# Kernel optimization log

Hardware: AMD Instinct MI355X
Metric: run time of the kernel (lower is better)

## Reference

```python
import jax, jax.numpy as jnp
import numpy as np

B, T, E, H = 2, 2048, 1024, 16
Dh = E // H  # head_size = 64


def setup_inputs() -> dict:
    key = jax.random.key(0)
    ks = jax.random.split(key, 6)
    s = E ** -0.5
    x = jax.random.normal(ks[0], (B, T, E), dtype=jnp.float32)
    Wq = jax.random.normal(ks[1], (H, E, Dh), dtype=jnp.float32) * s
    Wk = jax.random.normal(ks[2], (H, E, Dh), dtype=jnp.float32) * s
    Wv = jax.random.normal(ks[3], (H, E, Dh), dtype=jnp.float32) * s
    wo_w = jax.random.normal(ks[4], (E, E), dtype=jnp.float32) * s  # torch Linear weight [out,in]
    wo_b = jax.random.normal(ks[5], (E,), dtype=jnp.float32) * 0.01
    return {"x": x, "Wq": Wq, "Wk": Wk, "Wv": Wv, "wo_w": wo_w, "wo_b": wo_b}


def reference(x, Wq, Wk, Wv, wo_w, wo_b):
    # Batched equivalent of the per-head Python loop: project all heads at once.
    q = jnp.einsum('bte,hed->bhtd', x, Wq)
    k = jnp.einsum('bte,hed->bhtd', x, Wk)
    v = jnp.einsum('bte,hed->bhtd', x, Wv)
    scale = Dh ** -0.5
    scores = jnp.einsum('bhtd,bhsd->bhts', q, k) * scale  # [B,H,T,T]
    causal = jnp.tril(jnp.ones((T, T), dtype=bool))
    scores = jnp.where(causal, scores, jnp.finfo(scores.dtype).min)
    att = jax.nn.softmax(scores, axis=-1)
    out = jnp.einsum('bhts,bhsd->bhtd', att, v)  # [B,H,T,Dh]
    # concat heads (head order along last dim, matching torch.cat over heads)
    out = out.transpose(0, 2, 1, 3).reshape(B, T, E)
    return out @ wo_w.T + wo_b
```

## Files before the change

### kernel.cpp

```cpp
#include <hip/hip_runtime.h>

#define B_ 2
#define T_ 2048
#define E_ 1024
#define H_ 16
#define DH 64

typedef unsigned short u16;
typedef unsigned int u32;
typedef __bf16 bf16x8 __attribute__((ext_vector_type(8)));
typedef float f32x4 __attribute__((ext_vector_type(4)));
typedef float f32x16 __attribute__((ext_vector_type(16)));

__device__ __forceinline__ u16 f2bf(float f) {
  u32 u = __builtin_bit_cast(u32, f);
  u = u + 0x7FFFu + ((u >> 16) & 1u);
  return (u16)(u >> 16);
}
__device__ __forceinline__ bf16x8 ldfrag(const u16* p) { return *(const bf16x8*)p; }

__device__ __forceinline__ void gload_lds16(const u16* g, u16* l) {
  __builtin_amdgcn_global_load_lds((const __attribute__((address_space(1))) u32*)g,
                                   (__attribute__((address_space(3))) u32*)l, 16, 0, 0);
}

__global__ __launch_bounds__(256) void k_conv_all(const float* __restrict__ x,
                                                  const float* __restrict__ Wq,
                                                  const float* __restrict__ Wk,
                                                  const float* __restrict__ Wv,
                                                  const float* __restrict__ wo_w,
                                                  u16* __restrict__ xb, u16* __restrict__ wT,
                                                  u16* __restrict__ woB) {
  __shared__ __align__(16) u16 Ls[64][68];
  const int t = threadIdx.x;
  const int bx = blockIdx.x;
  if (bx < 2048 || bx >= 2816) {
    const float* src = (bx < 2048) ? x : wo_w;
    u16* dst = (bx < 2048) ? xb : woB;
    u32 i = (((bx < 2048) ? bx : (bx - 2816)) * 256u + t) * 8u;
    float4 a = *(const float4*)(src + i);
    float4 b = *(const float4*)(src + i + 4);
    uint4 v;
    v.x = (u32)f2bf(a.x) | ((u32)f2bf(a.y) << 16);
    v.y = (u32)f2bf(a.z) | ((u32)f2bf(a.w) << 16);
    v.z = (u32)f2bf(b.x) | ((u32)f2bf(b.y) << 16);
    v.w = (u32)f2bf(b.z) | ((u32)f2bf(b.w) << 16);
    *(uint4*)(dst + i) = v;
    return;
  }
  const int idx = bx - 2048;
  const int e0 = (idx & 15) * 64;
  const int h = (idx >> 4) & 15;
  const int which = idx >> 8;
  const float* src = (which == 0) ? Wq : ((which == 1) ? Wk : Wv);
  const float scale = (which == 0) ? 0.18033688011112042f : 1.0f;
#pragma unroll
  for (int p = 0; p < 4; p++) {
    int id2 = p * 256 + t;
    int row = id2 >> 4, ch = id2 & 15;
    float4 v = *(const float4*)(src + ((size_t)h * E_ + e0 + row) * DH + ch * 4);
    uint2 pk;
    pk.x = (u32)f2bf(v.x * scale) | ((u32)f2bf(v.y * scale) << 16);
    pk.y = (u32)f2bf(v.z * scale) | ((u32)f2bf(v.w * scale) << 16);
    *(uint2*)(&Ls[row][ch * 4]) = pk;
  }
  __syncthreads();
  u16* dst = wT + ((size_t)which * H_ + h) * (DH * E_);
#pragma unroll
  for (int p = 0; p < 4; p++) {
    int id2 = p * 256 + t;
    int d = id2 >> 4, ec = id2 & 15;
    uint2 pk;
    pk.x = (u32)Ls[ec * 4 + 0][d] | ((u32)Ls[ec * 4 + 1][d] << 16);
    pk.y = (u32)Ls[ec * 4 + 2][d] | ((u32)Ls[ec * 4 + 3][d] << 16);
    *(uint2*)(dst + (size_t)d * E_ + e0 + ec * 4) = pk;
  }
}

__global__ __launch_bounds__(256, 3) void k_qkv(const u16* __restrict__ xb, const u16* __restrict__ wT,
                                                u16* __restrict__ Qb, u16* __restrict__ Kb,
                                                u16* __restrict__ VbT) {
  __shared__ __align__(16) u16 As[128 * 64];
  __shared__ __align__(16) u16 Bs[128 * 64];
  const int tid = threadIdx.x;
  const int w = tid >> 6, lane = tid & 63, quad = lane >> 4, lr = lane & 15;
  const int wr = w >> 1, wc = w & 1;
  const int bid = blockIdx.x;
  const int xcd = bid & 7, bidx = bid >> 3;
  const int t0 = (xcd * 4 + bidx / 24) * 128;
  const int n0 = (bidx % 24) * 128;
  const int sr = lane >> 3, sc = lane & 7;

  f32x4 acc[4][4];
  const f32x4 z4 = {0.f, 0.f, 0.f, 0.f};
#pragma unroll
  for (int i = 0; i < 4; i++)
#pragma unroll
    for (int j = 0; j < 4; j++) acc[i][j] = z4;

  for (int k0 = 0; k0 < E_; k0 += 64) {
    __syncthreads();
#pragma unroll
    for (int ii = 0; ii < 4; ii++) {
      int ra = w * 32 + ii * 8 + sr;
      gload_lds16(xb + (size_t)(t0 + ra) * E_ + k0 + ((sc ^ (ra & 7)) << 3),
                  As + (w * 32 + ii * 8) * 64);
      gload_lds16(wT + (size_t)(n0 + ra) * E_ + k0 + ((sc ^ (ra & 7)) << 3),
                  Bs + (w * 32 + ii * 8) * 64);
    }
    __syncthreads();
#pragma unroll
    for (int kk = 0; kk < 2; kk++) {
      bf16x8 af[4], bfv[4];
#pragma unroll
      for (int rt = 0; rt < 4; rt++) {
        int row = wr * 64 + rt * 16 + lr;
        af[rt] = ldfrag(As + row * 64 + (((kk * 4 + quad) ^ (row & 7)) << 3));
      }
#pragma unroll
      for (int ct = 0; ct < 4; ct++) {
        int row = wc * 64 + ct * 16 + lr;
        bfv[ct] = ldfrag(Bs + row * 64 + (((kk * 4 + quad) ^ (row & 7)) << 3));
      }
#pragma unroll
      for (int rt = 0; rt < 4; rt++)
#pragma unroll
        for (int ct = 0; ct < 4; ct++)
          acc[rt][ct] = __builtin_amdgcn_mfma_f32_16x16x32_bf16(af[rt], bfv[ct], acc[rt][ct], 0, 0, 0);
    }
  }

  const int qkv = n0 >> 10;
  if (qkv < 2) {
    u16* outp = (qkv == 0) ? Qb : Kb;
#pragma unroll
    for (int rt = 0; rt < 4; rt++)
#pragma unroll
      for (int ct = 0; ct < 4; ct++) {
        int n = n0 + wc * 64 + ct * 16 + lr;
        int h = (n >> 6) & 15, d = n & 63;
#pragma unroll
        for (int r = 0; r < 4; r++) {
          int t = t0 + wr * 64 + rt * 16 + quad * 4 + r;
          int bb = t >> 11, tt = t & 2047;
          outp[(((size_t)bb * H_ + h) * T_ + tt) * DH + d] = f2bf(acc[rt][ct][r]);
        }
      }
  } else {
#pragma unroll
    for (int rt = 0; rt < 4; rt++)
#pragma unroll
      for (int ct = 0; ct < 4; ct++) {
        int n = n0 + wc * 64 + ct * 16 + lr;
        int h = (n >> 6) & 15, d = n & 63;
        int t = t0 + wr * 64 + rt * 16 + quad * 4;
        int bb = t >> 11, tt = t & 2047;
        uint2 pk;
        pk.x = (u32)f2bf(acc[rt][ct][0]) | ((u32)f2bf(acc[rt][ct][1]) << 16);
        pk.y = (u32)f2bf(acc[rt][ct][2]) | ((u32)f2bf(acc[rt][ct][3]) << 16);
        *(uint2*)(VbT + (((size_t)bb * H_ + h) * DH + d) * T_ + tt) = pk;
      }
  }
}

__global__ __launch_bounds__(256, 2) void k_attn(const u16* __restrict__ Qb, const u16* __restrict__ Kb,
                                                 const u16* __restrict__ VbT, u16* __restrict__ AO) {
  __shared__ __align__(16) u16 smem[8192];
  __shared__ float Ll[128];
  u16* Ks = smem;
  u16* Vts = smem + 4096;
  float* Lo = (float*)smem;

  const int tid = threadIdx.x;
  const int w = tid >> 6, lane = tid & 63;
  const int l31 = lane & 31, hi = lane >> 5;
  const int qhalf = w & 1, shalf = w >> 1;
  const int srow = lane >> 3, schunk = lane & 7;
  const int i = blockIdx.x;
  const int h = blockIdx.y, bb = blockIdx.z;
  const u16* qb = Qb + ((size_t)bb * H_ + h) * (size_t)(T_ * DH);
  const u16* kb = Kb + ((size_t)bb * H_ + h) * (size_t)(T_ * DH);
  const u16* vbT = VbT + ((size_t)bb * H_ + h) * (size_t)(T_ * DH);
  const float MFIX = 20.0f;

  for (int jb = 0; jb < 2; jb++) {
    const int qt = jb ? i : (31 - i);
    const int t0 = qt * 64;
    const int q_abs = t0 + qhalf * 32 + l31;

    const u16* qrow = qb + (size_t)q_abs * DH;
    bf16x8 bq[4];
#pragma unroll
    for (int ki = 0; ki < 4; ki++) bq[ki] = ldfrag(qrow + ki * 16 + hi * 8);

    f32x16 o0 = {}, o1 = {};
    float l_i = 0.f;

    for (int jt = 0; jt <= qt; jt++) {
      const int j0 = jt * 64;
      __syncthreads();
#pragma unroll
      for (int ii = 0; ii < 2; ii++) {
        int r = w * 16 + ii * 8 + srow;
        gload_lds16(kb + (size_t)(j0 + r) * DH + ((schunk ^ (r & 7)) << 3),
                    Ks + (w * 16 + ii * 8) * 64);
        gload_lds16(vbT + (size_t)r * T_ + j0 + ((schunk ^ (r & 7)) << 3),
                    Vts + (w * 16 + ii * 8) * 64);
      }
      __syncthreads();

      f32x16 s_acc = {};
      const int krow = shalf * 32 + l31;
      __builtin_amdgcn_s_setprio(1);
#pragma unroll
      for (int ki = 0; ki < 4; ki++) {
        bf16x8 ak = ldfrag(Ks + krow * 64 + (((2 * ki + hi) ^ (krow & 7)) << 3));
        s_acc = __builtin_amdgcn_mfma_f32_32x32x16_bf16(ak, bq[ki], s_acc, 0, 0, 0);
      }
      __builtin_amdgcn_s_setprio(0);

      if (jt == qt) {
#pragma unroll
        for (int r16 = 0; r16 < 16; r16++) {
          int s_abs = j0 + shalf * 32 + (r16 & 3) + 8 * (r16 >> 2) + 4 * hi;
          if (s_abs > q_abs) s_acc[r16] = -__builtin_inff();
        }
      }

      float p[16];
      float rsum = 0.f;
#pragma unroll
      for (int r16 = 0; r16 < 16; r16++) {
        p[r16] = __builtin_amdgcn_exp2f(s_acc[r16] - MFIX);
        rsum += p[r16];
      }
      l_i += rsum;

      u32 a[8], xch[8];
#pragma unroll
      for (int g = 0; g < 8; g++)
        a[g] = (__builtin_bit_cast(u32, p[2 * g]) >> 16) |
               (__builtin_bit_cast(u32, p[2 * g + 1]) & 0xffff0000u);
#pragma unroll
      for (int g = 0; g < 8; g++) xch[g] = __shfl_xor(a[g], 32);

      __builtin_amdgcn_s_setprio(1);
#pragma unroll
      for (int ks = 0; ks < 2; ks++) {
        uint4 fu;
        fu.x = hi ? xch[4 * ks + 2] : a[4 * ks + 0];
        fu.y = hi ? xch[4 * ks + 3] : a[4 * ks + 1];
        fu.z = hi ? a[4 * ks + 2] : xch[4 * ks + 0];
        fu.w = hi ? a[4 * ks + 3] : xch[4 * ks + 1];
        bf16x8 bp = __builtin_bit_cast(bf16x8, fu);
        const int ch = shalf * 4 + ks * 2 + hi;
        {
          int vrow = l31;
          bf16x8 av = ldfrag(Vts + vrow * 64 + ((ch ^ (vrow & 7)) << 3));
          o0 = __builtin_amdgcn_mfma_f32_32x32x16_bf16(av, bp, o0, 0, 0, 0);
        }
        {
          int vrow = 32 + l31;
          bf16x8 av = ldfrag(Vts + vrow * 64 + ((ch ^ (vrow & 7)) << 3));
          o1 = __builtin_amdgcn_mfma_f32_32x32x16_bf16(av, bp, o1, 0, 0, 0);
        }
      }
      __builtin_amdgcn_s_setprio(0);
    }

    __syncthreads();
    if (shalf) {
      float* base = Lo + qhalf * 2048 + lane * 32;
#pragma unroll
      for (int g = 0; g < 4; g++) {
        float4 v = {o0[4 * g + 0], o0[4 * g + 1], o0[4 * g + 2], o0[4 * g + 3]};
        *(float4*)(base + ((g ^ (lane & 7)) << 2)) = v;
      }
#pragma unroll
      for (int g = 4; g < 8; g++) {
        float4 v = {o1[4 * g - 16], o1[4 * g - 15], o1[4 * g - 14], o1[4 * g - 13]};
        *(float4*)(base + ((g ^ (lane & 7)) << 2)) = v;
      }
      Ll[qhalf * 64 + lane] = l_i;
    }
    __syncthreads();
    if (!shalf) {
      float* base = Lo + qhalf * 2048 + lane * 32;
#pragma unroll
      for (int g = 0; g < 4; g++) {
        float4 v = *(float4*)(base + ((g ^ (lane & 7)) << 2));
        o0[4 * g + 0] += v.x; o0[4 * g + 1] += v.y;
        o0[4 * g + 2] += v.z; o0[4 * g + 3] += v.w;
      }
#pragma unroll
      for (int g = 4; g < 8; g++) {
        float4 v = *(float4*)(base + ((g ^ (lane & 7)) << 2));
        o1[4 * g - 16] += v.x; o1[4 * g - 15] += v.y;
        o1[4 * g - 14] += v.z; o1[4 * g - 13] += v.w;
      }
      l_i += Ll[qhalf * 64 + lane];
      l_i += __shfl_xor(l_i, 32);
      float inv = 1.0f / l_i;
      u16* orow = AO + ((size_t)bb * T_ + q_abs) * E_ + h * DH;
#pragma unroll
      for (int g = 0; g < 4; g++) {
        uint2 pk;
        pk.x = (u32)f2bf(o0[4 * g + 0] * inv) | ((u32)f2bf(o0[4 * g + 1] * inv) << 16);
        pk.y = (u32)f2bf(o0[4 * g + 2] * inv) | ((u32)f2bf(o0[4 * g + 3] * inv) << 16);
        *(uint2*)(orow + 8 * g + 4 * hi) = pk;
        pk.x = (u32)f2bf(o1[4 * g + 0] * inv) | ((u32)f2bf(o1[4 * g + 1] * inv) << 16);
        pk.y = (u32)f2bf(o1[4 * g + 2] * inv) | ((u32)f2bf(o1[4 * g + 3] * inv) << 16);
        *(uint2*)(orow + 32 + 8 * g + 4 * hi) = pk;
      }
    }
  }
}

__global__ __launch_bounds__(256, 3) void k_oproj(const u16* __restrict__ AO, const u16* __restrict__ woB,
                                                  const float* __restrict__ bias, float* __restrict__ out) {
  __shared__ __align__(16) u16 As[128 * 64];
  __shared__ __align__(16) u16 Bs[64 * 64];
  const int tid = threadIdx.x;
  const int w = tid >> 6, lane = tid & 63, quad = lane >> 4, lr = lane & 15;
  const int wr = w >> 1, wc = w & 1;
  const int bid = blockIdx.x;
  const int xcd = bid & 7, bidx = bid >> 3;
  const int r0 = (xcd * 4 + (bidx >> 4)) * 128;
  const int n0 = (bidx & 15) * 64;
  const int sr = lane >> 3, sc = lane & 7;

  f32x4 acc[4][2];
  const f32x4 z4 = {0.f, 0.f, 0.f, 0.f};
#pragma unroll
  for (int i = 0; i < 4; i++) {
    acc[i][0] = z4;
    acc[i][1] = z4;
  }

  for (int k0 = 0; k0 < E_; k0 += 64) {
    __syncthreads();
#pragma unroll
    for (int ii = 0; ii < 4; ii++) {
      int ra = w * 32 + ii * 8 + sr;
      gload_lds16(AO + (size_t)(r0 + ra) * E_ + k0 + ((sc ^ (ra & 7)) << 3),
                  As + (w * 32 + ii * 8) * 64);
    }
#pragma unroll
    for (int ii = 0; ii < 2; ii++) {
      int rb = w * 16 + ii * 8 + sr;
      gload_lds16(woB + (size_t)(n0 + rb) * E_ + k0 + ((sc ^ (rb & 7)) << 3),
                  Bs + (w * 16 + ii * 8) * 64);
    }
    __syncthreads();
#pragma unroll
    for (int kk = 0; kk < 2; kk++) {
      bf16x8 af[4], bfv[2];
#pragma unroll
      for (int rt = 0; rt < 4; rt++) {
        int row = wr * 64 + rt * 16 + lr;
        af[rt] = ldfrag(As + row * 64 + (((kk * 4 + quad) ^ (row & 7)) << 3));
      }
#pragma unroll
      for (int ct = 0; ct < 2; ct++) {
        int row = wc * 32 + ct * 16 + lr;
        bfv[ct] = ldfrag(Bs + row * 64 + (((kk * 4 + quad) ^ (row & 7)) << 3));
      }
#pragma unroll
      for (int rt = 0; rt < 4; rt++)
#pragma unroll
        for (int ct = 0; ct < 2; ct++)
          acc[rt][ct] = __builtin_amdgcn_mfma_f32_16x16x32_bf16(af[rt], bfv[ct], acc[rt][ct], 0, 0, 0);
    }
  }

#pragma unroll
  for (int ct = 0; ct < 2; ct++) {
    int col = n0 + wc * 32 + ct * 16 + lr;
    float bv = bias[col];
#pragma unroll
    for (int rt = 0; rt < 4; rt++)
#pragma unroll
      for (int r = 0; r < 4; r++) {
        int row = r0 + wr * 64 + rt * 16 + quad * 4 + r;
        out[(size_t)row * E_ + col] = acc[rt][ct][r] + bv;
      }
  }
}

extern "C" void kernel_launch(void* const* d_in, const int* in_sizes, int n_in,
                              void* d_out, int out_size, void* d_ws, size_t ws_size,
                              hipStream_t stream) {
  const float* x = (const float*)d_in[0];
  const float* Wq = (const float*)d_in[1];
  const float* Wk = (const float*)d_in[2];
  const float* Wv = (const float*)d_in[3];
  const float* wo_w = (const float*)d_in[4];
  const float* wo_b = (const float*)d_in[5];
  float* out = (float*)d_out;
  char* ws = (char*)d_ws;

  u16* xb  = (u16*)(ws + 0);
  u16* wT  = (u16*)(ws + 8388608);
  u16* woB = (u16*)(ws + 14680064);
  u16* Qb  = (u16*)(ws + 16777216);
  u16* Kb  = (u16*)(ws + 25165824);
  u16* VbT = (u16*)(ws + 33554432);
  u16* AO  = (u16*)(ws + 41943040);

  k_conv_all<<<3328, 256, 0, stream>>>(x, Wq, Wk, Wv, wo_w, xb, wT, woB);
  k_qkv<<<768, 256, 0, stream>>>(xb, wT, Qb, Kb, VbT);
  k_attn<<<dim3(16, 16, 2), 256, 0, stream>>>(Qb, Kb, VbT, AO);
  k_oproj<<<512, 256, 0, stream>>>(AO, woB, wo_b, out);
}
```

Measured before the change: 175.9 us.

## Load K/V fragments directly to registers with double buffering, XCD-aware block mapping

The attention kernel no longer stages K and V^T tiles through LDS with two barriers per tile. Each wave now loads its MFMA operand fragments straight from global memory into registers, double-buffered so the next tile's loads are issued before the current tile's compute. The launch also becomes a 1D grid whose blocks are mapped so that all blocks of a given (batch, head) land on the same XCD, aiming for better L2 reuse of K/V. The cost is more global and L2 traffic, since both qhalf waves reload the same fragments and the per-lane loads are less coalesced, plus higher register pressure from 16 extra bf16x8 registers.

```diff
diff --git a/kernel.cpp b/kernel.cpp
--- a/kernel.cpp
+++ b/kernel.cpp
@@ -165,23 +165,81 @@
 
 __global__ __launch_bounds__(256, 2) void k_attn(const u16* __restrict__ Qb, const u16* __restrict__ Kb,
                                                  const u16* __restrict__ VbT, u16* __restrict__ AO) {
-  __shared__ __align__(16) u16 smem[8192];
+  __shared__ __align__(16) float Lo[4096];
   __shared__ float Ll[128];
-  u16* Ks = smem;
-  u16* Vts = smem + 4096;
-  float* Lo = (float*)smem;
 
   const int tid = threadIdx.x;
   const int w = tid >> 6, lane = tid & 63;
   const int l31 = lane & 31, hi = lane >> 5;
   const int qhalf = w & 1, shalf = w >> 1;
-  const int srow = lane >> 3, schunk = lane & 7;
-  const int i = blockIdx.x;
-  const int h = blockIdx.y, bb = blockIdx.z;
+  const int bid = blockIdx.x;
+  const int xcd = bid & 7, kdec = bid >> 3;
+  const int hb = xcd * 4 + (kdec >> 4);
+  const int i = kdec & 15;
+  const int h = hb & 15, bb = hb >> 4;
   const u16* qb = Qb + ((size_t)bb * H_ + h) * (size_t)(T_ * DH);
-  const u16* kb = Kb + ((size_t)bb * H_ + h) * (size_t)(T_ * DH);
+  const u16* kbp = Kb + ((size_t)bb * H_ + h) * (size_t)(T_ * DH);
   const u16* vbT = VbT + ((size_t)bb * H_ + h) * (size_t)(T_ * DH);
   const float MFIX = 20.0f;
+
+  const u16* kfrag = kbp + (size_t)(shalf * 32 + l31) * DH + hi * 8;
+  const u16* vfrag0 = vbT + (size_t)l31 * T_ + shalf * 32 + hi * 8;
+  const u16* vfrag1 = vbT + (size_t)(32 + l31) * T_ + shalf * 32 + hi * 8;
+
+#define LOADT(K0, K1, K2, K3, V0, V1, V2, V3, J0)                        \
+  do {                                                                   \
+    const u16* kp_ = kfrag + (size_t)(J0) * DH;                          \
+    K0 = ldfrag(kp_); K1 = ldfrag(kp_ + 16);                             \
+    K2 = ldfrag(kp_ + 32); K3 = ldfrag(kp_ + 48);                        \
+    V0 = ldfrag(vfrag0 + (J0)); V1 = ldfrag(vfrag0 + (J0) + 16);         \
+    V2 = ldfrag(vfrag1 + (J0)); V3 = ldfrag(vfrag1 + (J0) + 16);         \
+  } while (0)
+
+#define COMPT(K0, K1, K2, K3, V0, V1, V2, V3, JT)                            \
+  do {                                                                       \
+    f32x16 s_acc = {};                                                       \
+    __builtin_amdgcn_s_setprio(1);                                           \
+    s_acc = __builtin_amdgcn_mfma_f32_32x32x16_bf16(K0, bq[0], s_acc, 0, 0, 0); \
+    s_acc = __builtin_amdgcn_mfma_f32_32x32x16_bf16(K1, bq[1], s_acc, 0, 0, 0); \
+    s_acc = __builtin_amdgcn_mfma_f32_32x32x16_bf16(K2, bq[2], s_acc, 0, 0, 0); \
+    s_acc = __builtin_amdgcn_mfma_f32_32x32x16_bf16(K3, bq[3], s_acc, 0, 0, 0); \
+    __builtin_amdgcn_s_setprio(0);                                           \
+    if ((JT) == qt) {                      \
+      _Pragma("unroll") for (int r16 = 0; r16 < 16; r16++) {                 \
+        int s_abs = (JT) * 64 + shalf * 32 + (r16 & 3) + 8 * (r16 >> 2) + 4 * hi; \
+        if (s_abs > q_abs) s_acc[r16] = -__builtin_inff();                   \
+      }                                                                      \
+    }                                                                        \
+    float p_[16]; float rsum_ = 0.f;                                         \
+    _Pragma("unroll") for (int r16 = 0; r16 < 16; r16++) {                   \
+      p_[r16] = __builtin_amdgcn_exp2f(s_acc[r16] - MFIX);                   \
+      rsum_ += p_[r16];                                                      \
+    }                                                                        \
+    l_i += rsum_;                                                            \
+    u32 a_[8], xch_[8];                                                      \
+    _Pragma("unroll") for (int g = 0; g < 8; g++)                            \
+      a_[g] = (__builtin_bit_cast(u32, p_[2 * g]) >> 16) |                   \
+              (__builtin_bit_cast(u32, p_[2 * g + 1]) & 0xffff0000u);        \
+    _Pragma("unroll") for (int g = 0; g < 8; g++) xch_[g] = __shfl_xor(a_[g], 32); \
+    __builtin_amdgcn_s_setprio(1);                                           \
+    {                                                                        \
+      uint4 fu;                                                              \
+      fu.x = hi ? xch_[2] : a_[0]; fu.y = hi ? xch_[3] : a_[1];              \
+      fu.z = hi ? a_[2] : xch_[0]; fu.w = hi ? a_[3] : xch_[1];              \
+      bf16x8 bp = __builtin_bit_cast(bf16x8, fu);                            \
+      o0 = __builtin_amdgcn_mfma_f32_32x32x16_bf16(V0, bp, o0, 0, 0, 0);     \
+      o1 = __builtin_amdgcn_mfma_f32_32x32x16_bf16(V2, bp, o1, 0, 0, 0);     \
+    }                                                                        \
+    {                                                                        \
+      uint4 fu;                                                              \
+      fu.x = hi ? xch_[6] : a_[4]; fu.y = hi ? xch_[7] : a_[5];              \
+      fu.z = hi ? a_[6] : xch_[4]; fu.w = hi ? a_[7] : xch_[5];              \
+      bf16x8 bp = __builtin_bit_cast(bf16x8, fu);                            \
+      o0 = __builtin_amdgcn_mfma_f32_32x32x16_bf16(V1, bp, o0, 0, 0, 0);     \
+      o1 = __builtin_amdgcn_mfma_f32_32x32x16_bf16(V3, bp, o1, 0, 0, 0);     \
+    }                                                                        \
+    __builtin_amdgcn_s_setprio(0);                                           \
+  } while (0)
 
   for (int jb = 0; jb < 2; jb++) {
     const int qt = jb ? i : (31 - i);
@@ -196,76 +254,20 @@
     f32x16 o0 = {}, o1 = {};
     float l_i = 0.f;
 
-    for (int jt = 0; jt <= qt; jt++) {
-      const int j0 = jt * 64;
-      __syncthreads();
-#pragma unroll
-      for (int ii = 0; ii < 2; ii++) {
-        int r = w * 16 + ii * 8 + srow;
-        gload_lds16(kb + (size_t)(j0 + r) * DH + ((schunk ^ (r & 7)) << 3),
-                    Ks + (w * 16 + ii * 8) * 64);
-        gload_lds16(vbT + (size_t)r * T_ + j0 + ((schunk ^ (r & 7)) << 3),
-                    Vts + (w * 16 + ii * 8) * 64);
-      }
-      __syncthreads();
-
-      f32x16 s_acc = {};
-      const int krow = shalf * 32 + l31;
-      __builtin_amdgcn_s_setprio(1);
-#pragma unroll
-      for (int ki = 0; ki < 4; ki++) {
-        bf16x8 ak = ldfrag(Ks + krow * 64 + (((2 * ki + hi) ^ (krow & 7)) << 3));
-        s_acc = __builtin_amdgcn_mfma_f32_32x32x16_bf16(ak, bq[ki], s_acc, 0, 0, 0);
-      }
-      __builtin_amdgcn_s_setprio(0);
-
-      if (jt == qt) {
-#pragma unroll
-        for (int r16 = 0; r16 < 16; r16++) {
-          int s_abs = j0 + shalf * 32 + (r16 & 3) + 8 * (r16 >> 2) + 4 * hi;
-          if (s_abs > q_abs) s_acc[r16] = -__builtin_inff();
-        }
-      }
-
-      float p[16];
-      float rsum = 0.f;
-#pragma unroll
-      for (int r16 = 0; r16 < 16; r16++) {
-        p[r16] = __builtin_amdgcn_exp2f(s_acc[r16] - MFIX);
-        rsum += p[r16];
-      }
-      l_i += rsum;
-
-      u32 a[8], xch[8];
-#pragma unroll
-      for (int g = 0; g < 8; g++)
-        a[g] = (__builtin_bit_cast(u32, p[2 * g]) >> 16) |
-               (__builtin_bit_cast(u32, p[2 * g + 1]) & 0xffff0000u);
-#pragma unroll
-      for (int g = 0; g < 8; g++) xch[g] = __shfl_xor(a[g], 32);
-
-      __builtin_amdgcn_s_setprio(1);
-#pragma unroll
-      for (int ks = 0; ks < 2; ks++) {
-        uint4 fu;
-        fu.x = hi ? xch[4 * ks + 2] : a[4 * ks + 0];
-        fu.y = hi ? xch[4 * ks + 3] : a[4 * ks + 1];
-        fu.z = hi ? a[4 * ks + 2] : xch[4 * ks + 0];
-        fu.w = hi ? a[4 * ks + 3] : xch[4 * ks + 1];
-        bf16x8 bp = __builtin_bit_cast(bf16x8, fu);
-        const int ch = shalf * 4 + ks * 2 + hi;
-        {
-          int vrow = l31;
-          bf16x8 av = ldfrag(Vts + vrow * 64 + ((ch ^ (vrow & 7)) << 3));
-          o0 = __builtin_amdgcn_mfma_f32_32x32x16_bf16(av, bp, o0, 0, 0, 0);
-        }
-        {
-          int vrow = 32 + l31;
-          bf16x8 av = ldfrag(Vts + vrow * 64 + ((ch ^ (vrow & 7)) << 3));
-          o1 = __builtin_amdgcn_mfma_f32_32x32x16_bf16(av, bp, o1, 0, 0, 0);
-        }
-      }
-      __builtin_amdgcn_s_setprio(0);
+    bf16x8 A0, A1, A2, A3, AV0, AV1, AV2, AV3;
+    bf16x8 B0, B1, B2, B3, BV0, BV1, BV2, BV3;
+
+    LOADT(A0, A1, A2, A3, AV0, AV1, AV2, AV3, 0);
+    int jt = 0;
+    while (true) {
+      if (jt + 1 <= qt) LOADT(B0, B1, B2, B3, BV0, BV1, BV2, BV3, (jt + 1) * 64);
+      COMPT(A0, A1, A2, A3, AV0, AV1, AV2, AV3, jt);
+      jt++;
+      if (jt > qt) break;
+      if (jt + 1 <= qt) LOADT(A0, A1, A2, A3, AV0, AV1, AV2, AV3, (jt + 1) * 64);
+      COMPT(B0, B1, B2, B3, BV0, BV1, BV2, BV3, jt);
+      jt++;
+      if (jt > qt) break;
     }
 
     __syncthreads();
@@ -314,6 +316,8 @@
       }
     }
   }
+#undef LOADT
+#undef COMPT
 }
 
 __global__ __launch_bounds__(256, 3) void k_oproj(const u16* __restrict__ AO, const u16* __restrict__ woB,
@@ -409,6 +413,6 @@
 
   k_conv_all<<<3328, 256, 0, stream>>>(x, Wq, Wk, Wv, wo_w, xb, wT, woB);
   k_qkv<<<768, 256, 0, stream>>>(xb, wT, Qb, Kb, VbT);
-  k_attn<<<dim3(16, 16, 2), 256, 0, stream>>>(Qb, Kb, VbT, AO);
+  k_attn<<<512, 256, 0, stream>>>(Qb, Kb, VbT, AO);
   k_oproj<<<512, 256, 0, stream>>>(AO, woB, wo_b, out);
 }
```

After: 192.4 us. 9.4% more time.
